# Kernel optimization log

Hardware: AMD Instinct MI355X
Metric: run time of the kernel (lower is better)

The kernel has to match this reference:

```python
import jax, jax.numpy as jnp
import numpy as np

B, H, W, C = 8, 64, 64, 64
C8 = C // 8

def setup_inputs() -> dict:
    key = jax.random.key(0)
    ks = jax.random.split(key, 5)
    x = jax.random.normal(ks[0], (B, H, W, C), dtype=jnp.float32)
    # 1x1 conv kernels (fan-in scaled) + biases
    wq = jax.random.normal(ks[1], (C, C8), dtype=jnp.float32) / np.sqrt(C)
    wk = jax.random.normal(ks[2], (C, C8), dtype=jnp.float32) / np.sqrt(C)
    wv = jax.random.normal(ks[3], (C, C), dtype=jnp.float32) / np.sqrt(C)
    bq = jnp.zeros((C8,), dtype=jnp.float32)
    bk = jnp.zeros((C8,), dtype=jnp.float32)
    bv = jnp.zeros((C,), dtype=jnp.float32)
    gamma = jax.random.normal(ks[4], (), dtype=jnp.float32)
    return {"x": x, "wq": wq, "bq": bq, "wk": wk, "bk": bk,
            "wv": wv, "bv": bv, "gamma": gamma}

def reference(x, wq, bq, wk, bk, wv, bv, gamma):
    b, h, w, c = x.shape
    n = h * w
    # 1x1 convs == per-pixel linear projections
    q = (jnp.einsum('bhwc,cd->bhwd', x, wq) + bq).reshape(b, n, -1)  # [B,N,C/8]
    k = (jnp.einsum('bhwc,cd->bhwd', x, wk) + bk).reshape(b, n, -1)  # [B,N,C/8]
    v = (jnp.einsum('bhwc,cd->bhwd', x, wv) + bv).reshape(b, n, -1)  # [B,N,C]
    # Unscaled attention: softmax over keys (last axis), no 1/sqrt(d)
    attn = jax.nn.softmax(jnp.einsum('bnd,bmd->bnm', q, k), axis=-1)  # [B,N,N]
    out = jnp.einsum('bnm,bmc->bnc', attn, v).reshape(b, h, w, c)
    return out * gamma + x
```

## Files before the change

kernel.cpp:

```cpp
#include <hip/hip_runtime.h>
#include <hip/hip_bf16.h>


#define BB 8
#define NN 4096
#define CC 64
#define PSTRIDE 72
#define LOG2E 1.44269504088896f

typedef _Float16 f16;
typedef _Float16 half8 __attribute__((ext_vector_type(8)));
typedef _Float16 half4 __attribute__((ext_vector_type(4)));
typedef __fp16 fp16x2 __attribute__((ext_vector_type(2)));
typedef float floatx4 __attribute__((ext_vector_type(4)));

static __device__ inline half4 pack4(float a, float b, float c, float d) {
    fp16x2 lo = __builtin_amdgcn_cvt_pkrtz(a, b);
    fp16x2 hi = __builtin_amdgcn_cvt_pkrtz(c, d);
    unsigned int lou = __builtin_bit_cast(unsigned int, lo);
    unsigned int hiu = __builtin_bit_cast(unsigned int, hi);
    unsigned long long packed = (unsigned long long)lou | ((unsigned long long)hiu << 32);
    return __builtin_bit_cast(half4, packed);
}


__global__ __launch_bounds__(256) void proj_all_kernel(
    const float* __restrict__ x,
    const float* __restrict__ wq, const float* __restrict__ bq,
    const float* __restrict__ wk, const float* __restrict__ bk,
    const float* __restrict__ wv, const float* __restrict__ bv,
    f16* __restrict__ Qh, f16* __restrict__ Kf, f16* __restrict__ Vf,
    float* __restrict__ qn2, float* __restrict__ Mk2)
{
    __shared__ alignas(16) f16 Ws[80][PSTRIDE];
    __shared__ float Bs[80];
    __shared__ alignas(16) f16 Vst[64][68];
    __shared__ alignas(16) f16 Ks[64][12];
    __shared__ float redK[4];
    const int tid = threadIdx.x;

    for (int i4 = tid; i4 < 1024; i4 += 256) {
        const int i = i4 * 4;
        const int cin = i >> 6, cout = i & 63;
        const float4 w = *(const float4*)(wv + i);
        Ws[cout + 0][cin] = (f16)w.x;
        Ws[cout + 1][cin] = (f16)w.y;
        Ws[cout + 2][cin] = (f16)w.z;
        Ws[cout + 3][cin] = (f16)w.w;
    }
    if (tid < 128) {
        const int i = tid * 4;
        const int cin = i >> 3, c = i & 7;
        const float4 a = *(const float4*)(wq + i);
        const float4 k = *(const float4*)(wk + i);
        Ws[64 + c + 0][cin] = (f16)(a.x * LOG2E);
        Ws[64 + c + 1][cin] = (f16)(a.y * LOG2E);
        Ws[64 + c + 2][cin] = (f16)(a.z * LOG2E);
        Ws[64 + c + 3][cin] = (f16)(a.w * LOG2E);
        Ws[72 + c + 0][cin] = (f16)k.x;
        Ws[72 + c + 1][cin] = (f16)k.y;
        Ws[72 + c + 2][cin] = (f16)k.z;
        Ws[72 + c + 3][cin] = (f16)k.w;
    }
    if (tid < 80)
        Bs[tid] = (tid < 64) ? bv[tid]
                : (tid < 72 ? bq[tid - 64] * LOG2E : bk[tid - 72]);
    __syncthreads();

    const int wave = tid >> 6, lane = tid & 63;
    const int quad = lane >> 4, n16 = lane & 15;
    const long pb = (long)blockIdx.x * 64;
    const long p0 = pb + wave * 16;
    const int  b   = (int)(pb >> 12);
    const int  nnb = (int)(pb & 4095);

    half8 ax[2];
#pragma unroll
    for (int kh = 0; kh < 2; ++kh) {
        const float* xp = x + (p0 + n16) * 64 + kh * 32 + quad * 8;
        float4 x1 = *(const float4*)xp;
        float4 x2 = *(const float4*)(xp + 4);
        ax[kh][0] = (f16)x1.x; ax[kh][1] = (f16)x1.y;
        ax[kh][2] = (f16)x1.z; ax[kh][3] = (f16)x1.w;
        ax[kh][4] = (f16)x2.x; ax[kh][5] = (f16)x2.y;
        ax[kh][6] = (f16)x2.z; ax[kh][7] = (f16)x2.w;
    }

#pragma unroll
    for (int ct = 0; ct < 5; ++ct) {
        const int cout = (ct < 4) ? ct * 16 + n16 : 64 + n16;
        const float bias = Bs[cout];
        half8 b0 = *(const half8*)(&Ws[cout][quad * 8]);
        half8 b1 = *(const half8*)(&Ws[cout][32 + quad * 8]);
        floatx4 acc = {bias, bias, bias, bias};
        acc = __builtin_amdgcn_mfma_f32_16x16x32_f16(ax[0], b0, acc, 0, 0, 0);
        acc = __builtin_amdgcn_mfma_f32_16x16x32_f16(ax[1], b1, acc, 0, 0, 0);
        if (ct < 4) {
            half4 vp = {(f16)acc[0], (f16)acc[1], (f16)acc[2], (f16)acc[3]};
            *(half4*)(&Vst[ct * 16 + n16][wave * 16 + quad * 4]) = vp;
        } else {
            float n2[4];
#pragma unroll
            for (int r = 0; r < 4; ++r) n2[r] = acc[r] * acc[r];
#pragma unroll
            for (int d = 1; d < 8; d <<= 1)
#pragma unroll
                for (int r = 0; r < 4; ++r) n2[r] += __shfl_xor(n2[r], d, 64);
            if (n16 == 0) {
#pragma unroll
                for (int r = 0; r < 4; ++r) qn2[p0 + quad * 4 + r] = n2[r];
            }
            float km = fmaxf(fmaxf(n2[0], n2[1]), fmaxf(n2[2], n2[3]));
            km = fmaxf(km, __shfl_xor(km, 16, 64));
            km = fmaxf(km, __shfl_xor(km, 32, 64));
            if (n16 == 8) redK[wave] = km;
            if (n16 < 8) {
                f16* dst = Qh + (p0 + quad * 4) * 8 + n16;
#pragma unroll
                for (int r = 0; r < 4; ++r) dst[r * 8] = (f16)acc[r];
            } else {
#pragma unroll
                for (int r = 0; r < 4; ++r)
                    Ks[wave * 16 + quad * 4 + r][n16 - 8] = (f16)acc[r];
            }
        }
    }
    __syncthreads();

    if (tid == 0) {
        float m = fmaxf(fmaxf(redK[0], redK[1]), fmaxf(redK[2], redK[3]));
        atomicMax((unsigned int*)&Mk2[b], __float_as_uint(m));
    }

#pragma unroll
    for (int u = 0; u < 2; ++u) {
        const int tt = wave * 2 + u;
        const int kb = tt >> 2, ct = tt & 3;
        half4 lo = *(const half4*)(&Vst[ct * 16 + n16][kb * 32 + quad * 4]);
        half4 hi = *(const half4*)(&Vst[ct * 16 + n16][kb * 32 + 16 + quad * 4]);
        half8 v = {lo[0], lo[1], lo[2], lo[3], hi[0], hi[1], hi[2], hi[3]};
        const size_t kbg = (size_t)b * 128 + (nnb >> 5) + kb;
        *(half8*)(Vf + (kbg * 4 + ct) * 512 + lane * 8) = v;
    }
    if (wave < 2) {
        half8 kp = {0, 0, 0, 0, 0, 0, 0, 0};
#pragma unroll
        for (int e = 0; e < 2; ++e) {
            const int t = wave * 2 + e;
            if (quad < 2) {
                half4 kd = *(const half4*)(&Ks[t * 16 + n16][quad * 4]);
                kp[e * 4 + 0] = kd[0]; kp[e * 4 + 1] = kd[1];
                kp[e * 4 + 2] = kd[2]; kp[e * 4 + 3] = kd[3];
            } else if (quad == 2) {
                kp[e * 4 + 0] = (f16)1.f;
            }
        }
        const size_t kpg = (size_t)b * 128 + (nnb >> 5) + wave;
        *(half8*)(Kf + kpg * 512 + lane * 8) = kp;
    }
}

__global__ __launch_bounds__(256, 3) void attn_kernel(
    const f16* __restrict__ Qh, const f16* __restrict__ Kf,
    const f16* __restrict__ Vf,
    const float* __restrict__ qn2, const float* __restrict__ Mk2,
    const float* __restrict__ x, const float* __restrict__ gptr,
    float* __restrict__ out)
{
    __shared__ alignas(16) char smem[30720];
    __shared__ float Ls[4][2][16];
    float* Obuf = (float*)smem;

    const int tid  = threadIdx.x;
    const int wave = tid >> 6, lane = tid & 63;
    const int quad = lane >> 4, n16 = lane & 15;
    const int ks = wave;

    const int b  = blockIdx.x & 7;
    const int qt = blockIdx.x >> 3;
    const size_t bN = (size_t)b * NN;

    const float mk2 = Mk2[b];

    half4 bq4[2];
#pragma unroll
    for (int qt2 = 0; qt2 < 2; ++qt2) {
        const int q = qt * 32 + qt2 * 16 + n16;
        const float mf = __builtin_sqrtf(qn2[bN + q] * mk2) - 12.0f;
        half4 v = {0, 0, 0, 0};
        if (quad < 2)
            v = *(const half4*)(Qh + (bN + q) * 8 + quad * 4);
        else if (quad == 2)
            v[0] = (f16)(-mf);
        bq4[qt2] = v;
    }

    floatx4 oacc[2][4];
#pragma unroll
    for (int qt2 = 0; qt2 < 2; ++qt2)
#pragma unroll
        for (int ct = 0; ct < 4; ++ct) oacc[qt2][ct] = (floatx4){0.f, 0.f, 0.f, 0.f};
    float l_loc[2] = {0.f, 0.f};

    const f16* kfb = Kf + ((size_t)b * 128 + ks * 32) * 512 + lane * 8;
    const f16* vfb = Vf + ((size_t)b * 128 + ks * 32) * 2048 + lane * 8;
    const floatx4 zero4 = {0.f, 0.f, 0.f, 0.f};

    half8 kkc0 = *(const half8*)(kfb + 0);
    half8 kkc1 = *(const half8*)(kfb + 512);

    for (int it = 0; it < 16; ++it) {
        half8 avp[2][4];
#pragma unroll
        for (int p = 0; p < 2; ++p)
#pragma unroll
            for (int ct = 0; ct < 4; ++ct)
                avp[p][ct] = *(const half8*)(vfb + ((size_t)(it * 2 + p) * 4 + ct) * 512);

        half4 ak[4];
        ak[0] = __builtin_shufflevector(kkc0, kkc0, 0, 1, 2, 3);
        ak[1] = __builtin_shufflevector(kkc0, kkc0, 4, 5, 6, 7);
        ak[2] = __builtin_shufflevector(kkc1, kkc1, 0, 1, 2, 3);
        ak[3] = __builtin_shufflevector(kkc1, kkc1, 4, 5, 6, 7);

        const int itn = (it < 15) ? it + 1 : 15;
        kkc0 = *(const half8*)(kfb + (size_t)itn * 1024);
        kkc1 = *(const half8*)(kfb + (size_t)itn * 1024 + 512);

#pragma unroll
        for (int qt2 = 0; qt2 < 2; ++qt2) {
            floatx4 sf[4];
#pragma unroll
            for (int t = 0; t < 4; ++t)
                sf[t] = __builtin_amdgcn_mfma_f32_16x16x16f16(ak[t], bq4[qt2], zero4, 0, 0, 0);

            half4 pk[4];
            float rst[4];
#pragma unroll
            for (int t = 0; t < 4; ++t) {
                float p0 = __builtin_exp2f(sf[t][0]);
                float p1 = __builtin_exp2f(sf[t][1]);
                float p2 = __builtin_exp2f(sf[t][2]);
                float p3 = __builtin_exp2f(sf[t][3]);
                rst[t] = (p0 + p1) + (p2 + p3);
                pk[t] = pack4(p0, p1, p2, p3);
            }
            l_loc[qt2] += (rst[0] + rst[1]) + (rst[2] + rst[3]);

#pragma unroll
            for (int t = 0; t < 4; ++t) {
                const int p = t >> 1;
#pragma unroll
                for (int ct = 0; ct < 4; ++ct) {
                    half4 va = (t & 1)
                        ? __builtin_shufflevector(avp[p][ct], avp[p][ct], 4, 5, 6, 7)
                        : __builtin_shufflevector(avp[p][ct], avp[p][ct], 0, 1, 2, 3);
                    oacc[qt2][ct] = __builtin_amdgcn_mfma_f32_16x16x16f16(va, pk[t], oacc[qt2][ct], 0, 0, 0);
                }
            }
        }
    }

    float l_run[2];
#pragma unroll
    for (int qt2 = 0; qt2 < 2; ++qt2) {
        float l = l_loc[qt2];
        l += __shfl_xor(l, 16, 64);
        l += __shfl_xor(l, 32, 64);
        l_run[qt2] = l;
    }

    __syncthreads();
    if (ks > 0) {
#pragma unroll
        for (int qt2 = 0; qt2 < 2; ++qt2) {
            if (quad == 0) Ls[ks][qt2][n16] = l_run[qt2];
            float* ob = Obuf + (size_t)(((ks - 1) * 2 + qt2) * 64 + lane) * 20;
#pragma unroll
            for (int ct = 0; ct < 4; ++ct)
                *(floatx4*)(ob + ct * 4) = oacc[qt2][ct];
        }
    }
    __syncthreads();
    if (ks == 0) {
        const float g = gptr[0];
#pragma unroll
        for (int qt2 = 0; qt2 < 2; ++qt2) {
            float l = l_run[qt2];
            float o[16];
#pragma unroll
            for (int ct = 0; ct < 4; ++ct)
#pragma unroll
                for (int r = 0; r < 4; ++r) o[ct * 4 + r] = oacc[qt2][ct][r];
#pragma unroll
            for (int p = 1; p < 4; ++p) {
                l += Ls[p][qt2][n16];
                const float* ob = Obuf + (size_t)(((p - 1) * 2 + qt2) * 64 + lane) * 20;
#pragma unroll
                for (int ct = 0; ct < 4; ++ct) {
                    floatx4 t = *(const floatx4*)(ob + ct * 4);
                    o[ct * 4 + 0] += t[0]; o[ct * 4 + 1] += t[1];
                    o[ct * 4 + 2] += t[2]; o[ct * 4 + 3] += t[3];
                }
            }
            const float scale = g / l;
            const int q = qt * 32 + qt2 * 16 + n16;
#pragma unroll
            for (int ct = 0; ct < 4; ++ct) {
                const size_t idx = (bN + q) * CC + ct * 16 + quad * 4;
                float4 xr = *(const float4*)(x + idx);
                float4 res;
                res.x = o[ct * 4 + 0] * scale + xr.x;
                res.y = o[ct * 4 + 1] * scale + xr.y;
                res.z = o[ct * 4 + 2] * scale + xr.z;
                res.w = o[ct * 4 + 3] * scale + xr.w;
                *(float4*)(out + idx) = res;
            }
        }
    }
}

extern "C" void kernel_launch(void* const* d_in, const int* in_sizes, int n_in,
                              void* d_out, int out_size, void* d_ws, size_t ws_size,
                              hipStream_t stream) {
    const float* x     = (const float*)d_in[0];
    const float* wq    = (const float*)d_in[1];
    const float* bq    = (const float*)d_in[2];
    const float* wk    = (const float*)d_in[3];
    const float* bk    = (const float*)d_in[4];
    const float* wv    = (const float*)d_in[5];
    const float* bv    = (const float*)d_in[6];
    const float* gamma = (const float*)d_in[7];
    float* out = (float*)d_out;

    f16* Qh = (f16*)d_ws;
    f16* Kf = Qh + (size_t)BB * NN * 8;
    f16* Vf = Kf + (size_t)BB * 128 * 512;
    float* qn2 = (float*)(Vf + (size_t)BB * 128 * 4 * 512);
    float* kn2 = qn2 + (size_t)BB * NN;
    float* Mk2 = kn2 + (size_t)BB * NN;

    hipMemsetAsync(Mk2, 0, BB * sizeof(float), stream);
    proj_all_kernel<<<512, 256, 0, stream>>>(x, wq, bq, wk, bk, wv, bv,
                                             Qh, Kf, Vf, qn2, Mk2);
    attn_kernel<<<BB * 128, 256, 0, stream>>>(Qh, Kf, Vf, qn2, Mk2, x, gamma, out);
}
```

Measured before the change: 125.9 us.

## Share K/V tiles across waves via double-buffered LDS with larger query blocks

Each block now handles 128 queries with each wave iterating over all keys, instead of splitting keys across waves and reducing partial outputs through shared memory. K and V tiles are loaded asynchronously into a double-buffered LDS staging area with global_load_lds so all four waves reuse them, cutting global/L2 traffic per query. The cross-wave reduction is removed, but the grid shrinks to 256 blocks with one block per CU, lowering occupancy and adding a barrier per iteration.

```diff
diff --git a/kernel.cpp b/kernel.cpp
--- a/kernel.cpp
+++ b/kernel.cpp
@@ -13,6 +13,11 @@
 typedef _Float16 half4 __attribute__((ext_vector_type(4)));
 typedef __fp16 fp16x2 __attribute__((ext_vector_type(2)));
 typedef float floatx4 __attribute__((ext_vector_type(4)));
+
+#define GLD16(gsrc, ldst) \
+    __builtin_amdgcn_global_load_lds( \
+        (const __attribute__((address_space(1))) void*)(gsrc), \
+        (__attribute__((address_space(3))) void*)(ldst), 16, 0, 0)
 
 static __device__ inline half4 pack4(float a, float b, float c, float d) {
     fp16x2 lo = __builtin_amdgcn_cvt_pkrtz(a, b);
@@ -160,24 +165,21 @@
     }
 }
 
-__global__ __launch_bounds__(256, 3) void attn_kernel(
+__global__ __launch_bounds__(256, 1) void attn_kernel(
     const f16* __restrict__ Qh, const f16* __restrict__ Kf,
     const f16* __restrict__ Vf,
     const float* __restrict__ qn2, const float* __restrict__ Mk2,
     const float* __restrict__ x, const float* __restrict__ gptr,
     float* __restrict__ out)
 {
-    __shared__ alignas(16) char smem[30720];
-    __shared__ float Ls[4][2][16];
-    float* Obuf = (float*)smem;
+    __shared__ alignas(16) f16 KVb[2][10][512];
 
     const int tid  = threadIdx.x;
     const int wave = tid >> 6, lane = tid & 63;
     const int quad = lane >> 4, n16 = lane & 15;
-    const int ks = wave;
 
     const int b  = blockIdx.x & 7;
-    const int qt = blockIdx.x >> 3;
+    const int qb = blockIdx.x >> 3;
     const size_t bN = (size_t)b * NN;
 
     const float mk2 = Mk2[b];
@@ -185,7 +187,7 @@
     half4 bq4[2];
 #pragma unroll
     for (int qt2 = 0; qt2 < 2; ++qt2) {
-        const int q = qt * 32 + qt2 * 16 + n16;
+        const int q = qb * 128 + wave * 32 + qt2 * 16 + n16;
         const float mf = __builtin_sqrtf(qn2[bN + q] * mk2) - 12.0f;
         half4 v = {0, 0, 0, 0};
         if (quad < 2)
@@ -202,30 +204,54 @@
         for (int ct = 0; ct < 4; ++ct) oacc[qt2][ct] = (floatx4){0.f, 0.f, 0.f, 0.f};
     float l_loc[2] = {0.f, 0.f};
 
-    const f16* kfb = Kf + ((size_t)b * 128 + ks * 32) * 512 + lane * 8;
-    const f16* vfb = Vf + ((size_t)b * 128 + ks * 32) * 2048 + lane * 8;
+    const f16* kfb = Kf + (size_t)b * 128 * 512;
+    const f16* vfb = Vf + (size_t)b * 128 * 2048;
     const floatx4 zero4 = {0.f, 0.f, 0.f, 0.f};
-
-    half8 kkc0 = *(const half8*)(kfb + 0);
-    half8 kkc1 = *(const half8*)(kfb + 512);
-
-    for (int it = 0; it < 16; ++it) {
+    const int lo8 = lane * 8;
+
+    auto stage = [&](int bufi, int it) {
+        const size_t pr = (size_t)it * 2;
+        const f16* vs = vfb + pr * 2048 + lo8;
+        const f16* ks = kfb + pr * 512 + lo8;
+        f16 (*L)[512] = KVb[bufi];
+        if (wave == 0) {
+            GLD16(vs + 0 * 512, &L[0][0]);
+            GLD16(vs + 1 * 512, &L[1][0]);
+            GLD16(ks,           &L[8][0]);
+        } else if (wave == 1) {
+            GLD16(vs + 2 * 512, &L[2][0]);
+            GLD16(vs + 3 * 512, &L[3][0]);
+            GLD16(ks + 512,     &L[9][0]);
+        } else if (wave == 2) {
+            GLD16(vs + 4 * 512, &L[4][0]);
+            GLD16(vs + 5 * 512, &L[5][0]);
+        } else {
+            GLD16(vs + 6 * 512, &L[6][0]);
+            GLD16(vs + 7 * 512, &L[7][0]);
+        }
+    };
+
+    stage(0, 0);
+
+    for (int it = 0; it < 64; ++it) {
+        __syncthreads();
+        if (it < 63) stage((it + 1) & 1, it + 1);
+
+        const f16 (*L)[512] = KVb[it & 1];
+        half8 kk0 = *(const half8*)(&L[8][lo8]);
+        half8 kk1 = *(const half8*)(&L[9][lo8]);
         half8 avp[2][4];
 #pragma unroll
         for (int p = 0; p < 2; ++p)
 #pragma unroll
             for (int ct = 0; ct < 4; ++ct)
-                avp[p][ct] = *(const half8*)(vfb + ((size_t)(it * 2 + p) * 4 + ct) * 512);
+                avp[p][ct] = *(const half8*)(&L[p * 4 + ct][lo8]);
 
         half4 ak[4];
-        ak[0] = __builtin_shufflevector(kkc0, kkc0, 0, 1, 2, 3);
-        ak[1] = __builtin_shufflevector(kkc0, kkc0, 4, 5, 6, 7);
-        ak[2] = __builtin_shufflevector(kkc1, kkc1, 0, 1, 2, 3);
-        ak[3] = __builtin_shufflevector(kkc1, kkc1, 4, 5, 6, 7);
-
-        const int itn = (it < 15) ? it + 1 : 15;
-        kkc0 = *(const half8*)(kfb + (size_t)itn * 1024);
-        kkc1 = *(const half8*)(kfb + (size_t)itn * 1024 + 512);
+        ak[0] = __builtin_shufflevector(kk0, kk0, 0, 1, 2, 3);
+        ak[1] = __builtin_shufflevector(kk0, kk0, 4, 5, 6, 7);
+        ak[2] = __builtin_shufflevector(kk1, kk1, 0, 1, 2, 3);
+        ak[3] = __builtin_shufflevector(kk1, kk1, 4, 5, 6, 7);
 
 #pragma unroll
         for (int qt2 = 0; qt2 < 2; ++qt2) {
@@ -261,61 +287,24 @@
         }
     }
 
-    float l_run[2];
+    const float g = gptr[0];
 #pragma unroll
     for (int qt2 = 0; qt2 < 2; ++qt2) {
         float l = l_loc[qt2];
         l += __shfl_xor(l, 16, 64);
         l += __shfl_xor(l, 32, 64);
-        l_run[qt2] = l;
-    }
-
-    __syncthreads();
-    if (ks > 0) {
-#pragma unroll
-        for (int qt2 = 0; qt2 < 2; ++qt2) {
-            if (quad == 0) Ls[ks][qt2][n16] = l_run[qt2];
-            float* ob = Obuf + (size_t)(((ks - 1) * 2 + qt2) * 64 + lane) * 20;
-#pragma unroll
-            for (int ct = 0; ct < 4; ++ct)
-                *(floatx4*)(ob + ct * 4) = oacc[qt2][ct];
-        }
-    }
-    __syncthreads();
-    if (ks == 0) {
-        const float g = gptr[0];
-#pragma unroll
-        for (int qt2 = 0; qt2 < 2; ++qt2) {
-            float l = l_run[qt2];
-            float o[16];
-#pragma unroll
-            for (int ct = 0; ct < 4; ++ct)
-#pragma unroll
-                for (int r = 0; r < 4; ++r) o[ct * 4 + r] = oacc[qt2][ct][r];
-#pragma unroll
-            for (int p = 1; p < 4; ++p) {
-                l += Ls[p][qt2][n16];
-                const float* ob = Obuf + (size_t)(((p - 1) * 2 + qt2) * 64 + lane) * 20;
-#pragma unroll
-                for (int ct = 0; ct < 4; ++ct) {
-                    floatx4 t = *(const floatx4*)(ob + ct * 4);
-                    o[ct * 4 + 0] += t[0]; o[ct * 4 + 1] += t[1];
-                    o[ct * 4 + 2] += t[2]; o[ct * 4 + 3] += t[3];
-                }
-            }
-            const float scale = g / l;
-            const int q = qt * 32 + qt2 * 16 + n16;
-#pragma unroll
-            for (int ct = 0; ct < 4; ++ct) {
-                const size_t idx = (bN + q) * CC + ct * 16 + quad * 4;
-                float4 xr = *(const float4*)(x + idx);
-                float4 res;
-                res.x = o[ct * 4 + 0] * scale + xr.x;
-                res.y = o[ct * 4 + 1] * scale + xr.y;
-                res.z = o[ct * 4 + 2] * scale + xr.z;
-                res.w = o[ct * 4 + 3] * scale + xr.w;
-                *(float4*)(out + idx) = res;
-            }
+        const float scale = g / l;
+        const int q = qb * 128 + wave * 32 + qt2 * 16 + n16;
+#pragma unroll
+        for (int ct = 0; ct < 4; ++ct) {
+            const size_t idx = (bN + q) * CC + ct * 16 + quad * 4;
+            float4 xr = *(const float4*)(x + idx);
+            float4 res;
+            res.x = oacc[qt2][ct][0] * scale + xr.x;
+            res.y = oacc[qt2][ct][1] * scale + xr.y;
+            res.z = oacc[qt2][ct][2] * scale + xr.z;
+            res.w = oacc[qt2][ct][3] * scale + xr.w;
+            *(float4*)(out + idx) = res;
         }
     }
 }
@@ -343,5 +332,5 @@
     hipMemsetAsync(Mk2, 0, BB * sizeof(float), stream);
     proj_all_kernel<<<512, 256, 0, stream>>>(x, wq, bq, wk, bk, wv, bv,
                                              Qh, Kf, Vf, qn2, Mk2);
-    attn_kernel<<<BB * 128, 256, 0, stream>>>(Qh, Kf, Vf, qn2, Mk2, x, gamma, out);
+    attn_kernel<<<BB * 32, 256, 0, stream>>>(Qh, Kf, Vf, qn2, Mk2, x, gamma, out);
 }
```

Measured after the change: 147.4 us. 1.17x slower.
